# Optimization experiments

Hardware: AMD Instinct MI355X
Metric: run time of the kernel (lower is better)

## Reference

```python
import jax, jax.numpy as jnp
import numpy as np

B, T, D, H = 4, 2048, 1024, 16
HD = D // H  # head_dim = 64

def setup_inputs() -> dict:
    key = jax.random.key(0)
    k1, k2, k3 = jax.random.split(key, 3)
    x = jax.random.normal(k1, (B, T, D), dtype=jnp.float32)
    Wqkv = jax.random.normal(k2, (D, 3 * D), dtype=jnp.float32) * (D ** -0.5)
    Wout = jax.random.normal(k3, (D, D), dtype=jnp.float32) * (D ** -0.5)
    return {"x": x, "Wqkv": Wqkv, "Wout": Wout}

def reference(x, Wqkv, Wout):
    Bb, Tt, C = x.shape
    qkv = x @ Wqkv  # [B,T,3D]
    qkv = qkv.reshape(Bb, Tt, 3, H, HD)
    q, k, v = qkv[:, :, 0], qkv[:, :, 1], qkv[:, :, 2]  # each [B,T,H,HD]
    scale = 1.0 / np.sqrt(HD)
    # scores [B,H,T,T]
    attn = jnp.einsum('bqhd,bkhd->bhqk', q, k) * scale
    causal = jnp.tril(jnp.ones((Tt, Tt), dtype=bool))
    attn = jnp.where(causal[None, None], attn, -jnp.inf)
    attn = jax.nn.softmax(attn, axis=-1)
    out = jnp.einsum('bhqk,bkhd->bqhd', attn, v).reshape(Bb, Tt, C)
    return out @ Wout
```

## Files before the change

kernel.cpp:

```cpp
#include <hip/hip_runtime.h>
#include <hip/hip_bf16.h>

#define T_SEQ 2048
#define NBATCH 4
#define NHEAD 16
#define HDIM 64
#define DMODEL 1024

typedef __bf16 bf16x8 __attribute__((ext_vector_type(8)));
typedef float f32x4 __attribute__((ext_vector_type(4)));
typedef float f32x16 __attribute__((ext_vector_type(16)));

__device__ __forceinline__ unsigned short f2bf(float f) {
  unsigned int u = __builtin_bit_cast(unsigned int, f);
  u += 0x7fffu + ((u >> 16) & 1u);
  return (unsigned short)(u >> 16);
}

__device__ __forceinline__ float fexp2(float x) {
  float r;
  asm("v_exp_f32 %0, %1" : "=v"(r) : "v"(x));
  return r;
}

__device__ __forceinline__ void async_cp16(void* lds, const void* g) {
  __builtin_amdgcn_global_load_lds((const __attribute__((address_space(1))) void*)g,
                                   (__attribute__((address_space(3))) void*)lds,
                                   16, 0, 0);
}

__global__ __launch_bounds__(256) void conv_bf16_k(const float* __restrict__ in,
                                                   unsigned short* __restrict__ out, int n) {
  int i = (blockIdx.x * 256 + threadIdx.x) * 4;
  if (i >= n) return;
  float4 v = *(const float4*)(in + i);
  ushort4 o;
  o.x = f2bf(v.x); o.y = f2bf(v.y); o.z = f2bf(v.z); o.w = f2bf(v.w);
  *(ushort4*)(out + i) = o;
}

__global__ __launch_bounds__(256) void transpose_bf16_k(const float* __restrict__ in,
                                                        unsigned short* __restrict__ out,
                                                        int R, int C) {
  __shared__ float tile[32][33];
  int c0 = blockIdx.x * 32, r0 = blockIdx.y * 32;
  int tx = threadIdx.x, ty = threadIdx.y;
#pragma unroll
  for (int j = 0; j < 32; j += 8)
    tile[ty + j][tx] = in[(size_t)(r0 + ty + j) * C + c0 + tx];
  __syncthreads();
#pragma unroll
  for (int j = 0; j < 32; j += 8)
    out[(size_t)(c0 + ty + j) * R + r0 + tx] = f2bf(tile[tx][ty + j]);
}

__global__ __launch_bounds__(512, 2) void gemm1_8ph_k(const unsigned short* __restrict__ A,
                                                      const unsigned short* __restrict__ Bt,
                                                      unsigned short* __restrict__ Qb,
                                                      unsigned short* __restrict__ Kb,
                                                      unsigned short* __restrict__ Vt) {
  __shared__ uint4 ldsv[8192];
  char* lds = (char*)ldsv;
  const int t = threadIdx.x;
  const int w = t >> 6, lane = t & 63;
  const int lr = lane & 15, lg = lane >> 4;
  const int wr = w >> 2, wc = w & 3;
  const int bid = blockIdx.x;
  const int wid = (bid & 7) * 48 + (bid >> 3);
  const int m0 = (wid / 12) * 256, n0 = (wid % 12) * 256;

  const int row0 = t >> 3;
  const int colc0 = (t & 7) ^ (row0 & 7);
  const int stU = w * 1024;

  const unsigned short* Abase = A + (size_t)(m0 + row0) * 1024 + colc0 * 8;
  const unsigned short* Bbase = Bt + (size_t)(n0 + row0) * 1024 + colc0 * 8;

#define STG(dst, base, h, kt)                                                   \
  {                                                                             \
    const unsigned short* _s = (base) + (size_t)(h) * 128 * 1024 + (kt) * 64;   \
    async_cp16(lds + (dst) + stU, _s);                                          \
    async_cp16(lds + (dst) + stU + 8192, _s + 64 * 1024);                       \
  }

  f32x4 acc[8][4];
#pragma unroll
  for (int mi = 0; mi < 8; ++mi)
#pragma unroll
    for (int ni = 0; ni < 4; ++ni) acc[mi][ni] = (f32x4){0.f, 0.f, 0.f, 0.f};

  STG(0, Abase, 0, 0);
  STG(16384, Abase, 1, 0);
  STG(32768, Bbase, 0, 0);
  STG(49152, Bbase, 1, 0);
  STG(65536 + 32768, Bbase, 0, 1);
  STG(65536 + 49152, Bbase, 1, 1);
  asm volatile("s_waitcnt vmcnt(4)" ::: "memory");
  __builtin_amdgcn_s_barrier();
  __builtin_amdgcn_sched_barrier(0);

  bf16x8 bfr[4][2], af[2][2];
  const int ldsA0 = wr * 16384;
  const int ldsB0 = 32768 + (wc >> 1) * 16384;
  const int brow = (wc & 1) * 64;

#define LDB(pbase)                                                                   \
  {                                                                                  \
    _Pragma("unroll") for (int ni = 0; ni < 4; ++ni) _Pragma("unroll")               \
        for (int kk = 0; kk < 2; ++kk) {                                             \
      int rrow = brow + ni * 16 + lr;                                                \
      int cc = (kk * 4 + lg) ^ (lr & 7);                                             \
      bfr[ni][kk] = *(const bf16x8*)(lds + (pbase) + ldsB0 + rrow * 128 + cc * 16);  \
    }                                                                                \
  }
#define LDA(Q, pbase)                                                                \
  {                                                                                  \
    _Pragma("unroll") for (int m2 = 0; m2 < 2; ++m2) _Pragma("unroll")               \
        for (int kk = 0; kk < 2; ++kk) {                                             \
      int rrow = (2 * (Q) + m2) * 16 + lr;                                           \
      int cc = (kk * 4 + lg) ^ (lr & 7);                                             \
      af[m2][kk] = *(const bf16x8*)(lds + (pbase) + ldsA0 + rrow * 128 + cc * 16);   \
    }                                                                                \
  }
#define MM(Q)                                                                        \
  {                                                                                  \
    __builtin_amdgcn_s_setprio(1);                                                   \
    _Pragma("unroll") for (int m2 = 0; m2 < 2; ++m2) _Pragma("unroll")               \
        for (int kk = 0; kk < 2; ++kk) _Pragma("unroll") for (int ni = 0; ni < 4;    \
                                                              ++ni) acc[2 * (Q) +    \
                                                                        m2][ni] =    \
            __builtin_amdgcn_mfma_f32_16x16x32_bf16(af[m2][kk], bfr[ni][kk],         \
                                                    acc[2 * (Q) + m2][ni], 0, 0, 0); \
    __builtin_amdgcn_s_setprio(0);                                                   \
  }
#define BAR()                                                                        \
  {                                                                                  \
    __builtin_amdgcn_s_barrier();                                                    \
    __builtin_amdgcn_sched_barrier(0);                                               \
  }

  for (int I = 0; I < 8; ++I) {
    const int t1 = 2 * I + 1;
    const int t2 = (2 * I + 2 < 16) ? 2 * I + 2 : 15;
    const int t3 = (2 * I + 3 < 16) ? 2 * I + 3 : 15;
    LDB(0); LDA(0, 0); STG(65536, Abase, 0, t1); BAR(); MM(0); BAR();
    LDA(1, 0); STG(65536 + 16384, Abase, 1, t1); BAR(); MM(1); BAR();
    LDA(2, 0); STG(32768, Bbase, 0, t2); BAR(); MM(2); BAR();
    LDA(3, 0); STG(49152, Bbase, 1, t2); BAR(); MM(3);
    asm volatile("s_waitcnt vmcnt(4)" ::: "memory");
    BAR();
    LDB(65536); LDA(0, 65536); STG(0, Abase, 0, t2); BAR(); MM(0); BAR();
    LDA(1, 65536); STG(16384, Abase, 1, t2); BAR(); MM(1); BAR();
    LDA(2, 65536); STG(65536 + 32768, Bbase, 0, t3); BAR(); MM(2); BAR();
    LDA(3, 65536); STG(65536 + 49152, Bbase, 1, t3); BAR(); MM(3);
    asm volatile("s_waitcnt vmcnt(4)" ::: "memory");
    BAR();
  }

#pragma unroll
  for (int mi = 0; mi < 8; ++mi) {
#pragma unroll
    for (int ni = 0; ni < 4; ++ni) {
      int gm = m0 + wr * 128 + mi * 16 + lg * 4;
      int gn = n0 + wc * 64 + ni * 16 + lr;
      f32x4 v = acc[mi][ni];
      int b = gm >> 11, tt = gm & 2047;
      int sel = gn >> 10, rem = gn & 1023;
      int h = rem >> 6, hd = rem & 63;
      int bh = b * NHEAD + h;
      if (sel == 0) {
        unsigned short* p = Qb + ((size_t)bh * T_SEQ + tt) * HDIM + hd;
#pragma unroll
        for (int r = 0; r < 4; ++r) p[(size_t)r * HDIM] = f2bf(v[r] * (0.125f * 1.44269504f));
      } else if (sel == 1) {
        unsigned short* p = Kb + (size_t)bh * T_SEQ * HDIM + (tt >> 5) * 2048 +
                            (hd >> 4) * 512 + ((hd >> 3) & 1) * 256 + (tt & 31) * 8 +
                            (hd & 7);
#pragma unroll
        for (int r = 0; r < 4; ++r) p[r * 8] = f2bf(v[r]);
      } else {
        unsigned short* p = Vt + (size_t)bh * T_SEQ * HDIM + (tt >> 4) * 1024 +
                            ((tt >> 3) & 1) * 512 + (hd >> 5) * 256 + (hd & 31) * 8 +
                            (tt & 7);
        ushort4 o;
        o.x = f2bf(v[0]); o.y = f2bf(v[1]); o.z = f2bf(v[2]); o.w = f2bf(v[3]);
        *(ushort4*)p = o;
      }
    }
  }
#undef STG
#undef LDB
#undef LDA
#undef MM
#undef BAR
}

__global__ __launch_bounds__(256) void gemm_bt_k(const unsigned short* __restrict__ A,
                                                 const unsigned short* __restrict__ Bt,
                                                 int M, int N, int K,
                                                 float* __restrict__ Cout) {
  __shared__ unsigned short lA[128 * 32];
  __shared__ unsigned short lB[128 * 32];
  const int t = threadIdx.x;
  const int w = t >> 6, lane = t & 63;
  const int lr = lane & 15, lg = lane >> 4;
  const int wr = w >> 1, wc = w & 1;
  const int m0 = blockIdx.y * 128, n0 = blockIdx.x * 128;

  const f32x4 fzero = {0.f, 0.f, 0.f, 0.f};
  f32x4 acc[4][4];
#pragma unroll
  for (int mi = 0; mi < 4; ++mi)
#pragma unroll
    for (int ni = 0; ni < 4; ++ni) acc[mi][ni] = fzero;

  for (int k0 = 0; k0 < K; k0 += 32) {
    __syncthreads();
#pragma unroll
    for (int it = 0; it < 2; ++it) {
      int c = it * 256 + t;
      int row = c >> 2, kc = (c & 3) * 8;
      int cb = it * 256 + w * 64;
      async_cp16((char*)lA + cb * 16, A + (size_t)(m0 + row) * K + k0 + kc);
      async_cp16((char*)lB + cb * 16, Bt + (size_t)(n0 + row) * K + k0 + kc);
    }
    __syncthreads();
    bf16x8 af[4], bf[4];
#pragma unroll
    for (int mi = 0; mi < 4; ++mi)
      af[mi] = *(const bf16x8*)&lA[(wr * 64 + mi * 16 + lr) * 32 + lg * 8];
#pragma unroll
    for (int ni = 0; ni < 4; ++ni)
      bf[ni] = *(const bf16x8*)&lB[(wc * 64 + ni * 16 + lr) * 32 + lg * 8];
#pragma unroll
    for (int mi = 0; mi < 4; ++mi)
#pragma unroll
      for (int ni = 0; ni < 4; ++ni)
        acc[mi][ni] = __builtin_amdgcn_mfma_f32_16x16x32_bf16(af[mi], bf[ni], acc[mi][ni], 0, 0, 0);
  }

#pragma unroll
  for (int mi = 0; mi < 4; ++mi) {
#pragma unroll
    for (int ni = 0; ni < 4; ++ni) {
      int gm = m0 + wr * 64 + mi * 16 + lg * 4;
      int gn = n0 + wc * 64 + ni * 16 + lr;
      f32x4 v = acc[mi][ni];
#pragma unroll
      for (int r = 0; r < 4; ++r) Cout[(size_t)(gm + r) * N + gn] = v[r];
    }
  }
}

#define PVJJ(Sv, B, JJ, Oa, Obb)                                                              \
  {                                                                                           \
    unsigned w0, w1, w2, w3;                                                                  \
    asm("v_cvt_pk_bf16_f32 %0, %1, %2" : "=v"(w0) : "v"(Sv[B + 0]), "v"(Sv[B + 1]));          \
    asm("v_cvt_pk_bf16_f32 %0, %1, %2" : "=v"(w1) : "v"(Sv[B + 2]), "v"(Sv[B + 3]));          \
    asm("v_cvt_pk_bf16_f32 %0, %1, %2" : "=v"(w2) : "v"(Sv[B + 4]), "v"(Sv[B + 5]));          \
    asm("v_cvt_pk_bf16_f32 %0, %1, %2" : "=v"(w3) : "v"(Sv[B + 6]), "v"(Sv[B + 7]));          \
    asm("v_permlane32_swap_b32 %0, %1" : "+v"(w0), "+v"(w2));                                 \
    asm("v_permlane32_swap_b32 %0, %1" : "+v"(w1), "+v"(w3));                                 \
    union { unsigned u[4]; bf16x8 v; } pf;                                                    \
    pf.u[0] = w0; pf.u[1] = w1; pf.u[2] = w2; pf.u[3] = w3;                                   \
    bf16x8 vfa = *(const bf16x8*)(bv + (JJ) * 2048 + hi * 1024 + lq * 16);                    \
    bf16x8 vfb = *(const bf16x8*)(bv + (JJ) * 2048 + hi * 1024 + lq * 16 + 512);              \
    __builtin_amdgcn_s_setprio(1);                                                            \
    Oa = __builtin_amdgcn_mfma_f32_32x32x16_bf16(vfa, pf.v, Oa, 0, 0, 0);                     \
    Obb = __builtin_amdgcn_mfma_f32_32x32x16_bf16(vfb, pf.v, Obb, 0, 0, 0);                   \
    __builtin_amdgcn_s_setprio(0);                                                            \
  }

__global__ __launch_bounds__(512, 2) void attn_fwd9_k(const unsigned short* __restrict__ Qb,
                                                      const unsigned short* __restrict__ Kb,
                                                      const unsigned short* __restrict__ Vt,
                                                      unsigned short* __restrict__ Ob) {
  __shared__ char lds[32768];
  const int tid = threadIdx.x;
  const int w = tid >> 6, lane = tid & 63;
  const int lq = lane & 31, hi = lane >> 5;
  const int bid = blockIdx.x;
  const int xcd = bid & 7, i = bid >> 3;
  const int bh = xcd * 8 + (i & 7);
  const int s = (i < 32) ? 7 - (i >> 3) : (i >> 3) - 4;
  const int qb = s * 8 + w;
  const int qw = qb * 32;
  const int P = 4 * (s + 1);

  const unsigned short* Qp = Qb + (size_t)bh * T_SEQ * HDIM;
  const char* Ksrc = (const char*)(Kb + (size_t)bh * T_SEQ * HDIM);
  const char* Vsrc = (const char*)(Vt + (size_t)bh * T_SEQ * HDIM);
  const int b = bh >> 4, h = bh & 15;

#define ASTG(bb, p)                                                                  \
  {                                                                                  \
    async_cp16(lds + (bb) * 16384 + w * 1024, Ksrc + (size_t)(p) * 8192 + tid * 16); \
    async_cp16(lds + (bb) * 16384 + 8192 + w * 1024,                                 \
               Vsrc + (size_t)(p) * 8192 + tid * 16);                                \
  }

  bf16x8 qf[4];
#pragma unroll
  for (int dj = 0; dj < 4; ++dj)
    qf[dj] = *(const bf16x8*)(Qp + (size_t)(qw + lq) * HDIM + dj * 16 + hi * 8);

  f32x16 O0, O1;
#pragma unroll
  for (int r = 0; r < 16; ++r) { O0[r] = 0.f; O1[r] = 0.f; }
  float m_run = -30000.0f, l_run = 0.f;

  auto smax_pair = [&](f32x16& S0, f32x16& S1) {
    float m8[8];
#pragma unroll
    for (int r = 0; r < 8; ++r)
      m8[r] = fmaxf(fmaxf(S0[r], S0[r + 8]), fmaxf(S1[r], S1[r + 8]));
#pragma unroll
    for (int r = 0; r < 4; ++r) m8[r] = fmaxf(m8[r], m8[r + 4]);
    float pmax = fmaxf(fmaxf(m8[0], m8[1]), fmaxf(m8[2], m8[3]));
    pmax = fmaxf(pmax, __shfl_xor(pmax, 32, 64));
    if (__any(pmax > m_run + 11.5f)) {
      float mn = fmaxf(m_run, pmax);
      float al = fexp2(m_run - mn);
      m_run = mn;
      l_run *= al;
#pragma unroll
      for (int r = 0; r < 16; ++r) { O0[r] *= al; O1[r] *= al; }
    }
#pragma unroll
    for (int r = 0; r < 16; ++r) {
      S0[r] = fexp2(S0[r] - m_run);
      S1[r] = fexp2(S1[r] - m_run);
    }
    float s8[8];
#pragma unroll
    for (int r = 0; r < 8; ++r) s8[r] = (S0[r] + S0[r + 8]) + (S1[r] + S1[r + 8]);
#pragma unroll
    for (int r = 0; r < 4; ++r) s8[r] += s8[r + 4];
    float ps = (s8[0] + s8[1]) + (s8[2] + s8[3]);
    ps += __shfl_xor(ps, 32, 64);
    l_run += ps;
  };

  auto smax_single = [&](f32x16& S0) {
    float m8[8];
#pragma unroll
    for (int r = 0; r < 8; ++r) m8[r] = fmaxf(S0[r], S0[r + 8]);
#pragma unroll
    for (int r = 0; r < 4; ++r) m8[r] = fmaxf(m8[r], m8[r + 4]);
    float pmax = fmaxf(fmaxf(m8[0], m8[1]), fmaxf(m8[2], m8[3]));
    pmax = fmaxf(pmax, __shfl_xor(pmax, 32, 64));
    if (__any(pmax > m_run + 11.5f)) {
      float mn = fmaxf(m_run, pmax);
      float al = fexp2(m_run - mn);
      m_run = mn;
      l_run *= al;
#pragma unroll
      for (int r = 0; r < 16; ++r) { O0[r] *= al; O1[r] *= al; }
    }
#pragma unroll
    for (int r = 0; r < 16; ++r) S0[r] = fexp2(S0[r] - m_run);
    float s8[8];
#pragma unroll
    for (int r = 0; r < 8; ++r) s8[r] = S0[r] + S0[r + 8];
#pragma unroll
    for (int r = 0; r < 4; ++r) s8[r] += s8[r + 4];
    float ps = (s8[0] + s8[1]) + (s8[2] + s8[3]);
    ps += __shfl_xor(ps, 32, 64);
    l_run += ps;
  };

  ASTG(0, 0);
  __syncthreads();

  for (int p = 0; p < P; ++p) {
    if (p + 1 < P) ASTG((p + 1) & 1, p + 1);
    const char* bk = lds + (p & 1) * 16384;
    const char* bv = bk + 8192;
    const int t0 = 2 * p, t1 = 2 * p + 1;
    if (t0 <= qb) {
      const bool v1 = (t1 <= qb);
      f32x16 S0, S1;
#pragma unroll
      for (int r = 0; r < 16; ++r) { S0[r] = 0.f; S1[r] = 0.f; }
      __builtin_amdgcn_s_setprio(1);
#pragma unroll
      for (int dj = 0; dj < 4; ++dj) {
        bf16x8 k0 = *(const bf16x8*)(bk + dj * 1024 + lane * 16);
        S0 = __builtin_amdgcn_mfma_f32_32x32x16_bf16(k0, qf[dj], S0, 0, 0, 0);
      }
      if (v1) {
#pragma unroll
        for (int dj = 0; dj < 4; ++dj) {
          bf16x8 k1 = *(const bf16x8*)(bk + 4096 + dj * 1024 + lane * 16);
          S1 = __builtin_amdgcn_mfma_f32_32x32x16_bf16(k1, qf[dj], S1, 0, 0, 0);
        }
      }
      __builtin_amdgcn_s_setprio(0);
      if (t0 == qb) {
#pragma unroll
        for (int r = 0; r < 16; ++r) {
          int kvl = (r & 3) + 8 * (r >> 2) + 4 * hi;
          S0[r] = (kvl > lq) ? -30000.0f : S0[r];
        }
      }
      if (v1 && t1 == qb) {
#pragma unroll
        for (int r = 0; r < 16; ++r) {
          int kvl = (r & 3) + 8 * (r >> 2) + 4 * hi;
          S1[r] = (kvl > lq) ? -30000.0f : S1[r];
        }
      }
      if (v1) {
        smax_pair(S0, S1);
        PVJJ(S0, 0, 0, O0, O1); PVJJ(S0, 8, 1, O0, O1);
        PVJJ(S1, 0, 2, O0, O1); PVJJ(S1, 8, 3, O0, O1);
      } else {
        smax_single(S0);
        PVJJ(S0, 0, 0, O0, O1); PVJJ(S0, 8, 1, O0, O1);
      }
    }
    __syncthreads();
  }

  const float linv = 1.0f / l_run;
  unsigned short* op = Ob + ((size_t)(b * T_SEQ + qw + lq)) * DMODEL + h * HDIM;
#pragma unroll
  for (int g = 0; g < 4; ++g) {
    ushort4 o;
    o.x = f2bf(O0[4 * g + 0] * linv);
    o.y = f2bf(O0[4 * g + 1] * linv);
    o.z = f2bf(O0[4 * g + 2] * linv);
    o.w = f2bf(O0[4 * g + 3] * linv);
    *(ushort4*)(op + 8 * g + 4 * hi) = o;
    ushort4 o2;
    o2.x = f2bf(O1[4 * g + 0] * linv);
    o2.y = f2bf(O1[4 * g + 1] * linv);
    o2.z = f2bf(O1[4 * g + 2] * linv);
    o2.w = f2bf(O1[4 * g + 3] * linv);
    *(ushort4*)(op + 32 + 8 * g + 4 * hi) = o2;
  }
#undef ASTG
}

extern "C" void kernel_launch(void* const* d_in, const int* in_sizes, int n_in,
                              void* d_out, int out_size, void* d_ws, size_t ws_size,
                              hipStream_t stream) {
  const float* x = (const float*)d_in[0];
  const float* Wqkv = (const float*)d_in[1];
  const float* Wout = (const float*)d_in[2];
  float* out = (float*)d_out;

  unsigned short* ws = (unsigned short*)d_ws;
  const size_t nx = (size_t)NBATCH * T_SEQ * DMODEL;
  unsigned short* xb    = ws;
  unsigned short* wqkvT = xb + nx;
  unsigned short* woutT = wqkvT + (size_t)3 * DMODEL * DMODEL;
  unsigned short* Qb    = woutT + (size_t)DMODEL * DMODEL;
  unsigned short* Kb    = Qb + nx;
  unsigned short* Vt    = Kb + nx;
  unsigned short* Ab    = Vt + nx;
  size_t need = 2ull * (5 * nx + 4ull * DMODEL * DMODEL);
  if (ws_size < need) return;

  conv_bf16_k<<<dim3((unsigned)(nx / 1024)), dim3(256), 0, stream>>>(x, xb, (int)nx);
  transpose_bf16_k<<<dim3(3 * DMODEL / 32, DMODEL / 32), dim3(32, 8), 0, stream>>>(
      Wqkv, wqkvT, DMODEL, 3 * DMODEL);
  transpose_bf16_k<<<dim3(DMODEL / 32, DMODEL / 32), dim3(32, 8), 0, stream>>>(
      Wout, woutT, DMODEL, DMODEL);
  gemm1_8ph_k<<<dim3(384), dim3(512), 0, stream>>>(xb, wqkvT, Qb, Kb, Vt);
  attn_fwd9_k<<<dim3(512), dim3(512), 0, stream>>>(Qb, Kb, Vt, Ab);
  gemm_bt_k<<<dim3(DMODEL / 128, NBATCH * T_SEQ / 128), dim3(256), 0, stream>>>(
      Ab, woutT, NBATCH * T_SEQ, DMODEL, DMODEL, out);
}
```

Baseline: 162.4 us.

## Unify QKV and output GEMMs into templated 256x128 pipelined kernel

Replaces the 256x256-tile QKV GEMM with a templated 256x128-tile, 8-wave pipelined kernel (double-buffered async LDS staging, 96KB LDS) that runs 768 blocks instead of 384. The same template, with a plain fp32 store epilogue, replaces the simple single-buffered output-projection GEMM. The aim is better wave balance across CUs for the QKV GEMM and a much stronger software pipeline for the Wout GEMM. The cost is lower per-block reuse and occupancy of one block per CU.

After: 155.9 us. -4.0%, faster.

```diff
diff --git a/kernel.cpp b/kernel.cpp
--- a/kernel.cpp
+++ b/kernel.cpp
@@ -54,20 +54,23 @@
     out[(size_t)(c0 + ty + j) * R + r0 + tx] = f2bf(tile[tx][ty + j]);
 }
 
-__global__ __launch_bounds__(512, 2) void gemm1_8ph_k(const unsigned short* __restrict__ A,
+template <int EPI, int NT>
+__global__ __launch_bounds__(512, 1) void gemm_8ph2_k(const unsigned short* __restrict__ A,
                                                       const unsigned short* __restrict__ Bt,
                                                       unsigned short* __restrict__ Qb,
                                                       unsigned short* __restrict__ Kb,
-                                                      unsigned short* __restrict__ Vt) {
-  __shared__ uint4 ldsv[8192];
+                                                      unsigned short* __restrict__ Vt,
+                                                      float* __restrict__ Cout) {
+  __shared__ uint4 ldsv[6144];
   char* lds = (char*)ldsv;
   const int t = threadIdx.x;
   const int w = t >> 6, lane = t & 63;
   const int lr = lane & 15, lg = lane >> 4;
-  const int wr = w >> 2, wc = w & 3;
+  const int wr = w >> 1, wc = w & 1;
   const int bid = blockIdx.x;
-  const int wid = (bid & 7) * 48 + (bid >> 3);
-  const int m0 = (wid / 12) * 256, n0 = (wid % 12) * 256;
+  const int perx = (NT * 32) / 8;
+  const int wid = (bid & 7) * perx + (bid >> 3);
+  const int m0 = (wid / NT) * 256, n0 = (wid % NT) * 128;
 
   const int row0 = t >> 3;
   const int colc0 = (t & 7) ^ (row0 & 7);
@@ -76,50 +79,59 @@
   const unsigned short* Abase = A + (size_t)(m0 + row0) * 1024 + colc0 * 8;
   const unsigned short* Bbase = Bt + (size_t)(n0 + row0) * 1024 + colc0 * 8;
 
-#define STG(dst, base, h, kt)                                                   \
+#define STGA(dst, h, kt)                                                        \
   {                                                                             \
-    const unsigned short* _s = (base) + (size_t)(h) * 128 * 1024 + (kt) * 64;   \
-    async_cp16(lds + (dst) + stU, _s);                                          \
-    async_cp16(lds + (dst) + stU + 8192, _s + 64 * 1024);                       \
-  }
-
-  f32x4 acc[8][4];
-#pragma unroll
-  for (int mi = 0; mi < 8; ++mi)
+    const unsigned short* _s = Abase + (size_t)(h) * 128 * 1024 + (kt) * 64;    \
+    async_cp16(lds + (dst) + (h) * 16384 + stU, _s);                            \
+    async_cp16(lds + (dst) + (h) * 16384 + stU + 8192, _s + 64 * 1024);         \
+  }
+#define STGB(dst, kt)                                                           \
+  {                                                                             \
+    const unsigned short* _s = Bbase + (kt) * 64;                               \
+    async_cp16(lds + (dst) + 32768 + stU, _s);                                  \
+    async_cp16(lds + (dst) + 32768 + stU + 8192, _s + 64 * 1024);               \
+  }
+#define VM2() asm volatile("s_waitcnt vmcnt(2)" ::: "memory")
+#define BAR()                                                                   \
+  {                                                                             \
+    __builtin_amdgcn_s_barrier();                                               \
+    __builtin_amdgcn_sched_barrier(0);                                          \
+  }
+
+  f32x4 acc[4][4];
+#pragma unroll
+  for (int mi = 0; mi < 4; ++mi)
 #pragma unroll
     for (int ni = 0; ni < 4; ++ni) acc[mi][ni] = (f32x4){0.f, 0.f, 0.f, 0.f};
 
-  STG(0, Abase, 0, 0);
-  STG(16384, Abase, 1, 0);
-  STG(32768, Bbase, 0, 0);
-  STG(49152, Bbase, 1, 0);
-  STG(65536 + 32768, Bbase, 0, 1);
-  STG(65536 + 49152, Bbase, 1, 1);
-  asm volatile("s_waitcnt vmcnt(4)" ::: "memory");
-  __builtin_amdgcn_s_barrier();
-  __builtin_amdgcn_sched_barrier(0);
+  STGA(0, 0, 0);
+  STGA(0, 1, 0);
+  STGB(0, 0);
+  STGB(49152, 1);
+  VM2();
+  BAR();
 
   bf16x8 bfr[4][2], af[2][2];
-  const int ldsA0 = wr * 16384;
-  const int ldsB0 = 32768 + (wc >> 1) * 16384;
-  const int brow = (wc & 1) * 64;
+  const int ldsAh = (wr >> 1) * 16384;
+  const int arow0 = (wr & 1) * 64;
+  const int brow0 = wc * 64;
 
 #define LDB(pbase)                                                                   \
   {                                                                                  \
     _Pragma("unroll") for (int ni = 0; ni < 4; ++ni) _Pragma("unroll")               \
         for (int kk = 0; kk < 2; ++kk) {                                             \
-      int rrow = brow + ni * 16 + lr;                                                \
+      int rrow = brow0 + ni * 16 + lr;                                               \
       int cc = (kk * 4 + lg) ^ (lr & 7);                                             \
-      bfr[ni][kk] = *(const bf16x8*)(lds + (pbase) + ldsB0 + rrow * 128 + cc * 16);  \
+      bfr[ni][kk] = *(const bf16x8*)(lds + (pbase) + 32768 + rrow * 128 + cc * 16);  \
     }                                                                                \
   }
 #define LDA(Q, pbase)                                                                \
   {                                                                                  \
     _Pragma("unroll") for (int m2 = 0; m2 < 2; ++m2) _Pragma("unroll")               \
         for (int kk = 0; kk < 2; ++kk) {                                             \
-      int rrow = (2 * (Q) + m2) * 16 + lr;                                           \
+      int rrow = arow0 + (2 * (Q) + m2) * 16 + lr;                                   \
       int cc = (kk * 4 + lg) ^ (lr & 7);                                             \
-      af[m2][kk] = *(const bf16x8*)(lds + (pbase) + ldsA0 + rrow * 128 + cc * 16);   \
+      af[m2][kk] = *(const bf16x8*)(lds + (pbase) + ldsAh + rrow * 128 + cc * 16);   \
     }                                                                                \
   }
 #define MM(Q)                                                                        \
@@ -133,110 +145,15 @@
                                                     acc[2 * (Q) + m2][ni], 0, 0, 0); \
     __builtin_amdgcn_s_setprio(0);                                                   \
   }
-#define BAR()                                                                        \
-  {                                                                                  \
-    __builtin_amdgcn_s_barrier();                                                    \
-    __builtin_amdgcn_sched_barrier(0);                                               \
-  }
 
   for (int I = 0; I < 8; ++I) {
-    const int t1 = 2 * I + 1;
-    const int t2 = (2 * I + 2 < 16) ? 2 * I + 2 : 15;
-    const int t3 = (2 * I + 3 < 16) ? 2 * I + 3 : 15;
-    LDB(0); LDA(0, 0); STG(65536, Abase, 0, t1); BAR(); MM(0); BAR();
-    LDA(1, 0); STG(65536 + 16384, Abase, 1, t1); BAR(); MM(1); BAR();
-    LDA(2, 0); STG(32768, Bbase, 0, t2); BAR(); MM(2); BAR();
-    LDA(3, 0); STG(49152, Bbase, 1, t2); BAR(); MM(3);
-    asm volatile("s_waitcnt vmcnt(4)" ::: "memory");
-    BAR();
-    LDB(65536); LDA(0, 65536); STG(0, Abase, 0, t2); BAR(); MM(0); BAR();
-    LDA(1, 65536); STG(16384, Abase, 1, t2); BAR(); MM(1); BAR();
-    LDA(2, 65536); STG(65536 + 32768, Bbase, 0, t3); BAR(); MM(2); BAR();
-    LDA(3, 65536); STG(65536 + 49152, Bbase, 1, t3); BAR(); MM(3);
-    asm volatile("s_waitcnt vmcnt(4)" ::: "memory");
-    BAR();
-  }
-
-#pragma unroll
-  for (int mi = 0; mi < 8; ++mi) {
-#pragma unroll
-    for (int ni = 0; ni < 4; ++ni) {
-      int gm = m0 + wr * 128 + mi * 16 + lg * 4;
-      int gn = n0 + wc * 64 + ni * 16 + lr;
-      f32x4 v = acc[mi][ni];
-      int b = gm >> 11, tt = gm & 2047;
-      int sel = gn >> 10, rem = gn & 1023;
-      int h = rem >> 6, hd = rem & 63;
-      int bh = b * NHEAD + h;
-      if (sel == 0) {
-        unsigned short* p = Qb + ((size_t)bh * T_SEQ + tt) * HDIM + hd;
-#pragma unroll
-        for (int r = 0; r < 4; ++r) p[(size_t)r * HDIM] = f2bf(v[r] * (0.125f * 1.44269504f));
-      } else if (sel == 1) {
-        unsigned short* p = Kb + (size_t)bh * T_SEQ * HDIM + (tt >> 5) * 2048 +
-                            (hd >> 4) * 512 + ((hd >> 3) & 1) * 256 + (tt & 31) * 8 +
-                            (hd & 7);
-#pragma unroll
-        for (int r = 0; r < 4; ++r) p[r * 8] = f2bf(v[r]);
-      } else {
-        unsigned short* p = Vt + (size_t)bh * T_SEQ * HDIM + (tt >> 4) * 1024 +
-                            ((tt >> 3) & 1) * 512 + (hd >> 5) * 256 + (hd & 31) * 8 +
-                            (tt & 7);
-        ushort4 o;
-        o.x = f2bf(v[0]); o.y = f2bf(v[1]); o.z = f2bf(v[2]); o.w = f2bf(v[3]);
-        *(ushort4*)p = o;
-      }
-    }
-  }
-#undef STG
-#undef LDB
-#undef LDA
-#undef MM
-#undef BAR
-}
-
-__global__ __launch_bounds__(256) void gemm_bt_k(const unsigned short* __restrict__ A,
-                                                 const unsigned short* __restrict__ Bt,
-                                                 int M, int N, int K,
-                                                 float* __restrict__ Cout) {
-  __shared__ unsigned short lA[128 * 32];
-  __shared__ unsigned short lB[128 * 32];
-  const int t = threadIdx.x;
-  const int w = t >> 6, lane = t & 63;
-  const int lr = lane & 15, lg = lane >> 4;
-  const int wr = w >> 1, wc = w & 1;
-  const int m0 = blockIdx.y * 128, n0 = blockIdx.x * 128;
-
-  const f32x4 fzero = {0.f, 0.f, 0.f, 0.f};
-  f32x4 acc[4][4];
-#pragma unroll
-  for (int mi = 0; mi < 4; ++mi)
-#pragma unroll
-    for (int ni = 0; ni < 4; ++ni) acc[mi][ni] = fzero;
-
-  for (int k0 = 0; k0 < K; k0 += 32) {
-    __syncthreads();
-#pragma unroll
-    for (int it = 0; it < 2; ++it) {
-      int c = it * 256 + t;
-      int row = c >> 2, kc = (c & 3) * 8;
-      int cb = it * 256 + w * 64;
-      async_cp16((char*)lA + cb * 16, A + (size_t)(m0 + row) * K + k0 + kc);
-      async_cp16((char*)lB + cb * 16, Bt + (size_t)(n0 + row) * K + k0 + kc);
-    }
-    __syncthreads();
-    bf16x8 af[4], bf[4];
-#pragma unroll
-    for (int mi = 0; mi < 4; ++mi)
-      af[mi] = *(const bf16x8*)&lA[(wr * 64 + mi * 16 + lr) * 32 + lg * 8];
-#pragma unroll
-    for (int ni = 0; ni < 4; ++ni)
-      bf[ni] = *(const bf16x8*)&lB[(wc * 64 + ni * 16 + lr) * 32 + lg * 8];
-#pragma unroll
-    for (int mi = 0; mi < 4; ++mi)
-#pragma unroll
-      for (int ni = 0; ni < 4; ++ni)
-        acc[mi][ni] = __builtin_amdgcn_mfma_f32_16x16x32_bf16(af[mi], bf[ni], acc[mi][ni], 0, 0, 0);
+    const int t1o = 2 * I + 1;
+    const int t2e = (2 * I + 2 < 16) ? 2 * I + 2 : 15;
+    const int t3o = (2 * I + 3 < 16) ? 2 * I + 3 : 15;
+    LDB(0); LDA(0, 0); STGA(49152, 0, t1o); BAR(); MM(0); BAR();
+    LDA(1, 0); STGA(49152, 1, t1o); STGB(0, t2e); BAR(); MM(1); VM2(); BAR();
+    LDB(49152); LDA(0, 49152); STGA(0, 0, t2e); BAR(); MM(0); BAR();
+    LDA(1, 49152); STGA(0, 1, t2e); STGB(49152, t3o); BAR(); MM(1); VM2(); BAR();
   }
 
 #pragma unroll
@@ -246,10 +163,43 @@
       int gm = m0 + wr * 64 + mi * 16 + lg * 4;
       int gn = n0 + wc * 64 + ni * 16 + lr;
       f32x4 v = acc[mi][ni];
-#pragma unroll
-      for (int r = 0; r < 4; ++r) Cout[(size_t)(gm + r) * N + gn] = v[r];
+      if (EPI == 0) {
+        int b = gm >> 11, tt = gm & 2047;
+        int sel = gn >> 10, rem = gn & 1023;
+        int h = rem >> 6, hd = rem & 63;
+        int bh = b * NHEAD + h;
+        if (sel == 0) {
+          unsigned short* p = Qb + ((size_t)bh * T_SEQ + tt) * HDIM + hd;
+#pragma unroll
+          for (int r = 0; r < 4; ++r)
+            p[(size_t)r * HDIM] = f2bf(v[r] * (0.125f * 1.44269504f));
+        } else if (sel == 1) {
+          unsigned short* p = Kb + (size_t)bh * T_SEQ * HDIM + (tt >> 5) * 2048 +
+                              (hd >> 4) * 512 + ((hd >> 3) & 1) * 256 + (tt & 31) * 8 +
+                              (hd & 7);
+#pragma unroll
+          for (int r = 0; r < 4; ++r) p[r * 8] = f2bf(v[r]);
+        } else {
+          unsigned short* p = Vt + (size_t)bh * T_SEQ * HDIM + (tt >> 4) * 1024 +
+                              ((tt >> 3) & 1) * 512 + (hd >> 5) * 256 + (hd & 31) * 8 +
+                              (tt & 7);
+          ushort4 o;
+          o.x = f2bf(v[0]); o.y = f2bf(v[1]); o.z = f2bf(v[2]); o.w = f2bf(v[3]);
+          *(ushort4*)p = o;
+        }
+      } else {
+#pragma unroll
+        for (int r = 0; r < 4; ++r) Cout[(size_t)(gm + r) * (NT * 128) + gn] = v[r];
+      }
     }
   }
+#undef STGA
+#undef STGB
+#undef VM2
+#undef BAR
+#undef LDB
+#undef LDA
+#undef MM
 }
 
 #define PVJJ(Sv, B, JJ, Oa, Obb)                                                              \
@@ -467,8 +417,8 @@
       Wqkv, wqkvT, DMODEL, 3 * DMODEL);
   transpose_bf16_k<<<dim3(DMODEL / 32, DMODEL / 32), dim3(32, 8), 0, stream>>>(
       Wout, woutT, DMODEL, DMODEL);
-  gemm1_8ph_k<<<dim3(384), dim3(512), 0, stream>>>(xb, wqkvT, Qb, Kb, Vt);
+  gemm_8ph2_k<0, 24><<<dim3(768), dim3(512), 0, stream>>>(xb, wqkvT, Qb, Kb, Vt, nullptr);
   attn_fwd9_k<<<dim3(512), dim3(512), 0, stream>>>(Qb, Kb, Vt, Ab);
-  gemm_bt_k<<<dim3(DMODEL / 128, NBATCH * T_SEQ / 128), dim3(256), 0, stream>>>(
-      Ab, woutT, NBATCH * T_SEQ, DMODEL, DMODEL, out);
-}
+  gemm_8ph2_k<1, 8><<<dim3(256), dim3(512), 0, stream>>>(Ab, woutT, nullptr, nullptr,
+                                                         nullptr, out);
+}
```
